# Kernel tuning notes

Measured on AMD Instinct MI355X. Metric: run time of the kernel, lower is better.

## Reference

```python
import jax, jax.numpy as jnp
import numpy as np

N, E = 50000, 800000
H, C_IN, C_HID, C_OUT = 4, 256, 64, 64
NEG_SLOPE = 0.2


def leaky_relu(x, s=NEG_SLOPE):
    return jnp.where(x >= 0, x, s * x)


def gat_conv(x, src, dst, W, att_src, att_dst, bias, n_nodes):
    # x: [N, F_in], W: [F_in, H*C], att_*: [1, H, C], bias: [H*C]
    Hh, Cc = att_src.shape[1], att_src.shape[2]
    h = (x @ W).reshape(n_nodes, Hh, Cc)            # [N, H, C]
    a_src = (h * att_src).sum(-1)                   # [N, H]
    a_dst = (h * att_dst).sum(-1)                   # [N, H]
    alpha = leaky_relu(a_src[src] + a_dst[dst])     # [E, H]
    # segment softmax over incoming edges of each destination node
    m = jax.ops.segment_max(alpha, dst, num_segments=n_nodes)   # [N, H]
    e = jnp.exp(alpha - m[dst])                     # [E, H]
    denom = jax.ops.segment_sum(e, dst, num_segments=n_nodes)   # [N, H]
    w = e / jnp.clip(denom, 1e-16)[dst]             # [E, H]
    out = jax.ops.segment_sum(w[:, :, None] * h[src], dst, num_segments=n_nodes)
    return out.reshape(n_nodes, Hh * Cc) + bias


def setup_inputs() -> dict:
    key = jax.random.key(0)
    ks = jax.random.split(key, 10)
    glorot = lambda k, shp: jax.random.normal(k, shp, jnp.float32) * np.sqrt(2.0 / (shp[0] + shp[-1]))
    return {
        "x": jax.random.normal(ks[0], (N, C_IN), jnp.float32),
        "edge_index": jax.random.randint(ks[1], (2, E), 0, N, jnp.int32),
        "W1": glorot(ks[2], (C_IN, H * C_HID)),
        "att_src1": glorot(ks[3], (1, H, C_HID)),
        "att_dst1": glorot(ks[4], (1, H, C_HID)),
        "b1": jnp.zeros((H * C_HID,), jnp.float32),
        "W2": glorot(ks[5], (H * C_HID, H * C_OUT)),
        "att_src2": glorot(ks[6], (1, H, C_OUT)),
        "att_dst2": glorot(ks[7], (1, H, C_OUT)),
        "b2": jnp.zeros((H * C_OUT,), jnp.float32),
    }


def reference(x, edge_index, W1, att_src1, att_dst1, b1, W2, att_src2, att_dst2, b2):
    n = x.shape[0]
    loops = jnp.arange(n, dtype=edge_index.dtype)
    src = jnp.concatenate([edge_index[0], loops])
    dst = jnp.concatenate([edge_index[1], loops])
    h1 = gat_conv(x, src, dst, W1, att_src1, att_dst1, b1, n)
    h1 = jax.nn.relu(h1)
    out = gat_conv(h1, src, dst, W2, att_src2, att_dst2, b2, n)
    return out
```

## Files before the change

kernel.cpp:

```cpp
#include <hip/hip_runtime.h>
#include <math.h>

#define NEG_SLOPE 0.2f

typedef __attribute__((ext_vector_type(8))) short bf16x8;
typedef __attribute__((ext_vector_type(4))) float f32x4;
typedef __attribute__((ext_vector_type(4))) unsigned short u16x4;
typedef __attribute__((ext_vector_type(8))) unsigned short u16x8;

static __device__ __forceinline__ f32x4 lky4(f32x4 v) {
    f32x4 r;
    r.x = v.x >= 0.f ? v.x : NEG_SLOPE * v.x;
    r.y = v.y >= 0.f ? v.y : NEG_SLOPE * v.y;
    r.z = v.z >= 0.f ? v.z : NEG_SLOPE * v.z;
    r.w = v.w >= 0.f ? v.w : NEG_SLOPE * v.w;
    return r;
}
static __device__ __forceinline__ f32x4 exp4(f32x4 v) {
    f32x4 r;
    r.x = __expf(v.x); r.y = __expf(v.y); r.z = __expf(v.z); r.w = __expf(v.w);
    return r;
}
static __device__ __forceinline__ float bf2f(unsigned short u) {
    return __uint_as_float(((unsigned int)u) << 16);
}
static __device__ __forceinline__ unsigned short f2bf_rne(float f) {
    unsigned int u = __float_as_uint(f);
    u += 0x7fffu + ((u >> 16) & 1u);
    return (unsigned short)(u >> 16);
}


__global__ void hist_kernel(const int* __restrict__ dst, int* __restrict__ counts, int E, int Nn) {
    int i = blockIdx.x * blockDim.x + threadIdx.x;
    int tot = E + Nn;
    if (i < tot) {
        int d = (i < E) ? dst[i] : (i - E);
        atomicAdd(&counts[d], 1);
    }
}

__global__ void scan1_kernel(const int* __restrict__ counts, int* __restrict__ partial,
                             int* __restrict__ blockSums, int Nn) {
    __shared__ int sh[1024];
    int b = blockIdx.x, t = threadIdx.x;
    int base = b * 1024;
    int orig[4];
    for (int r = 0; r < 4; r++) {
        int i = t + r * 256;
        int v = (base + i < Nn) ? counts[base + i] : 0;
        orig[r] = v;
        sh[i] = v;
    }
    __syncthreads();
    for (int off = 1; off < 1024; off <<= 1) {
        int vals[4];
        for (int r = 0; r < 4; r++) { int i = t + r * 256; vals[r] = (i >= off) ? sh[i - off] : 0; }
        __syncthreads();
        for (int r = 0; r < 4; r++) { int i = t + r * 256; sh[i] += vals[r]; }
        __syncthreads();
    }
    for (int r = 0; r < 4; r++) {
        int i = t + r * 256;
        if (base + i < Nn) partial[base + i] = sh[i] - orig[r];
    }
    if (t == 0) blockSums[b] = sh[1023];
}

__global__ void scan2_kernel(int* __restrict__ blockSums, int nb) {
    if (threadIdx.x == 0 && blockIdx.x == 0) {
        int s = 0;
        for (int i = 0; i < nb; i++) { int v = blockSums[i]; blockSums[i] = s; s += v; }
    }
}

__global__ void finalize_kernel(const int* __restrict__ partial, const int* __restrict__ blockOff,
                                int* __restrict__ row_ptr, int Nn, int Etot) {
    int i = blockIdx.x * blockDim.x + threadIdx.x;
    if (i < Nn) row_ptr[i] = partial[i] + blockOff[i >> 10];
    if (i == 0) row_ptr[Nn] = Etot;
}

__global__ void scatter_kernel(const int* __restrict__ srcE, const int* __restrict__ dstE,
                               const int* __restrict__ row_ptr, int* __restrict__ fill,
                               int* __restrict__ srcs, int E, int Nn) {
    int i = blockIdx.x * blockDim.x + threadIdx.x;
    int tot = E + Nn;
    if (i < tot) {
        int s, d;
        if (i < E) { s = srcE[i]; d = dstE[i]; }
        else       { s = d = i - E; }
        int pos = row_ptr[d] + atomicAdd(&fill[d], 1);
        srcs[pos] = s;
    }
}

__global__ void convertA_kernel(const float* __restrict__ X, unsigned short* __restrict__ Ab,
                                int rows) {
    int t = blockIdx.x * 256 + threadIdx.x;
    if (t >= rows * 64) return;
    int r = t >> 6, c4 = t & 63;
    f32x4 v = *((const f32x4*)(X + ((size_t)r << 8)) + c4);
    u16x4 o;
    o.x = f2bf_rne(v.x); o.y = f2bf_rne(v.y);
    o.z = f2bf_rne(v.z); o.w = f2bf_rne(v.w);
    *(u16x4*)(Ab + (size_t)r * 256 + c4 * 4) = o;
}

__global__ void transposeW_kernel(const float* __restrict__ W, unsigned short* __restrict__ Bt) {
    int t = blockIdx.x * 256 + threadIdx.x;
    int n = t >> 8, k = t & 255;
    Bt[(size_t)n * 256 + k] = f2bf_rne(W[k * 256 + n]);
}

__global__ __launch_bounds__(256) void gemm_kernel(const unsigned short* __restrict__ Ab,
                                                   const unsigned short* __restrict__ Bt,
                                                   unsigned short* __restrict__ Gb,
                                                   int rows) {
    __shared__ __align__(128) unsigned char smem[65536];

    int tid = threadIdx.x;
    int lane = tid & 63, wid = tid >> 6;
    int wr = wid >> 1, wc = wid & 1;
    int bm = blockIdx.x * 128;
    int bn = blockIdx.y * 128;

    f32x4 zero4 = {0.f, 0.f, 0.f, 0.f};
    f32x4 acc[4][4];
#pragma unroll
    for (int i = 0; i < 4; i++)
#pragma unroll
        for (int j = 0; j < 4; j++) acc[i][j] = zero4;

    int sr = tid >> 3;
    int sc = tid & 7;

    auto stage = [&](int kt, int buf) {
        unsigned short* As = (unsigned short*)(smem + buf * 32768);
        unsigned short* Bs = As + 8192;
#pragma unroll
        for (int q = 0; q < 4; q++) {
            int rt = q * 32 + sr;
            int gr = bm + rt; if (gr >= rows) gr = rows - 1;
            int cg = sc ^ (rt & 7);
            const unsigned short* gp = Ab + (size_t)gr * 256 + kt + cg * 8;
            unsigned short* lp = As + rt * 64 + sc * 8;
            __builtin_amdgcn_global_load_lds(
                (__attribute__((address_space(1))) void*)(uintptr_t)gp,
                (__attribute__((address_space(3))) void*)lp, 16, 0, 0);
        }
#pragma unroll
        for (int q = 0; q < 4; q++) {
            int rt = q * 32 + sr;
            int gn = bn + rt;
            int cg = sc ^ (rt & 7);
            const unsigned short* gp = Bt + (size_t)gn * 256 + kt + cg * 8;
            unsigned short* lp = Bs + rt * 64 + sc * 8;
            __builtin_amdgcn_global_load_lds(
                (__attribute__((address_space(1))) void*)(uintptr_t)gp,
                (__attribute__((address_space(3))) void*)lp, 16, 0, 0);
        }
    };

    stage(0, 0);
    __syncthreads();

    for (int kt = 0; kt < 4; kt++) {
        if (kt < 3) stage((kt + 1) * 64, (kt + 1) & 1);
        unsigned short* As = (unsigned short*)(smem + (kt & 1) * 32768);
        unsigned short* Bs = As + 8192;
#pragma unroll
        for (int ks = 0; ks < 2; ks++) {
            bf16x8 af[4], bfr[4];
#pragma unroll
            for (int f = 0; f < 4; f++) {
                int r = wr * 64 + f * 16 + (lane & 15);
                int c = (ks * 4 + (lane >> 4)) ^ (r & 7);
                af[f] = *(const bf16x8*)(As + r * 64 + c * 8);
                int rb = wc * 64 + f * 16 + (lane & 15);
                int cb = (ks * 4 + (lane >> 4)) ^ (rb & 7);
                bfr[f] = *(const bf16x8*)(Bs + rb * 64 + cb * 8);
            }
#pragma unroll
            for (int i = 0; i < 4; i++)
#pragma unroll
                for (int j = 0; j < 4; j++)
                    acc[i][j] = __builtin_amdgcn_mfma_f32_16x16x32_bf16(af[i], bfr[j], acc[i][j], 0, 0, 0);
        }
        __syncthreads();
    }

    int r0 = wr * 64 + (lane >> 4) * 4;
    int c0 = wc * 64 + (lane & 15);
#pragma unroll
    for (int i = 0; i < 4; i++) {
#pragma unroll
        for (int j = 0; j < 4; j++) {
#pragma unroll
            for (int rg = 0; rg < 4; rg++) {
                int lr = bm + r0 + i * 16 + rg;
                if (lr < rows) {
                    int col = bn + c0 + j * 16;
                    Gb[(size_t)lr * 256 + col] = f2bf_rne(acc[i][j][rg]);
                }
            }
        }
    }
}

__global__ __launch_bounds__(256) void attn_kernel(const unsigned short* __restrict__ Gb,
                                                   const float* __restrict__ att_s,
                                                   const float* __restrict__ att_d,
                                                   float* __restrict__ a_src,
                                                   float* __restrict__ a_dst, int N) {
    int wv = threadIdx.x >> 6, lane = threadIdx.x & 63;
    int n = blockIdx.x * 4 + wv;
    if (n >= N) return;
    u16x4 g4 = *(const u16x4*)(Gb + (size_t)n * 256 + lane * 4);
    f32x4 g;
    g.x = bf2f(g4.x); g.y = bf2f(g4.y); g.z = bf2f(g4.z); g.w = bf2f(g4.w);
    f32x4 s4 = ((const f32x4*)att_s)[lane];
    f32x4 d4 = ((const f32x4*)att_d)[lane];
    f32x4 p = g * s4, q = g * d4;
    float ps = p.x + p.y + p.z + p.w;
    float pd = q.x + q.y + q.z + q.w;
#pragma unroll
    for (int off = 1; off < 16; off <<= 1) {
        ps += __shfl_xor(ps, off);
        pd += __shfl_xor(pd, off);
    }
    if ((lane & 15) == 0) {
        int head = lane >> 4;
        a_src[n * 4 + head] = ps;
        a_dst[n * 4 + head] = pd;
    }
}

__global__ __launch_bounds__(256) void wts_kernel(const float* __restrict__ a_src,
                                                  const float* __restrict__ a_dst,
                                                  const int* __restrict__ row_ptr,
                                                  const int* __restrict__ srcs,
                                                  float* __restrict__ wts, int N) {
    int wv = threadIdx.x >> 6, lane = threadIdx.x & 63;
    int n = blockIdx.x * 4 + wv;
    if (n >= N) return;
    int start = row_ptr[n], end = row_ptr[n + 1];
    const f32x4* as4p = (const f32x4*)a_src;
    f32x4 adn4 = *(const f32x4*)(a_dst + (size_t)n * 4);

    f32x4 zero = {0.f, 0.f, 0.f, 0.f};
    f32x4 ev0 = zero;
    int e0 = start + lane;
    if (e0 < end) {
        int s = srcs[e0];
        ev0 = exp4(lky4(as4p[s] + adn4));
    }
    f32x4 denom4 = ev0;
    for (int c0 = start + 64; c0 < end; c0 += 64) {
        int e = c0 + lane;
        if (e < end) {
            int s = srcs[e];
            denom4 += exp4(lky4(as4p[s] + adn4));
        }
    }
#pragma unroll
    for (int off = 32; off; off >>= 1) {
        denom4.x += __shfl_xor(denom4.x, off);
        denom4.y += __shfl_xor(denom4.y, off);
        denom4.z += __shfl_xor(denom4.z, off);
        denom4.w += __shfl_xor(denom4.w, off);
    }
    f32x4 rd;
    rd.x = 1.0f / denom4.x; rd.y = 1.0f / denom4.y;
    rd.z = 1.0f / denom4.z; rd.w = 1.0f / denom4.w;

    if (e0 < end) ((f32x4*)wts)[e0] = ev0 * rd;
    for (int c0 = start + 64; c0 < end; c0 += 64) {
        int e = c0 + lane;
        if (e < end) {
            int s = srcs[e];
            ((f32x4*)wts)[e] = exp4(lky4(as4p[s] + adn4)) * rd;
        }
    }
}

__global__ __launch_bounds__(256) void gather_kernel(const unsigned short* __restrict__ Gb,
                                                     const float* __restrict__ wts,
                                                     const int* __restrict__ row_ptr,
                                                     const int* __restrict__ srcs,
                                                     const float* __restrict__ bias,
                                                     float* __restrict__ outF,
                                                     unsigned short* __restrict__ outB,
                                                     int N) {
    int wv = threadIdx.x >> 6, lane = threadIdx.x & 63;
    int n = blockIdx.x * 4 + wv;
    if (n >= N) return;
    int half = lane >> 5;
    int sl = lane & 31;
    int head = sl >> 3;

    int start = row_ptr[n], end = row_ptr[n + 1];

    float acc[8] = {0.f, 0.f, 0.f, 0.f, 0.f, 0.f, 0.f, 0.f};

    int e = start + half;
    for (; e + 2 < end; e += 4) {
        int s0 = srcs[e];
        int s1 = srcs[e + 2];
        float w0 = wts[e * 4 + head];
        float w1 = wts[(e + 2) * 4 + head];
        u16x8 g0 = *(const u16x8*)(Gb + (size_t)s0 * 256 + sl * 8);
        u16x8 g1 = *(const u16x8*)(Gb + (size_t)s1 * 256 + sl * 8);
#pragma unroll
        for (int k = 0; k < 8; k++) {
            acc[k] = fmaf(bf2f(g0[k]), w0, acc[k]);
            acc[k] = fmaf(bf2f(g1[k]), w1, acc[k]);
        }
    }
    for (; e < end; e += 2) {
        int s0 = srcs[e];
        float w0 = wts[e * 4 + head];
        u16x8 g0 = *(const u16x8*)(Gb + (size_t)s0 * 256 + sl * 8);
#pragma unroll
        for (int k = 0; k < 8; k++)
            acc[k] = fmaf(bf2f(g0[k]), w0, acc[k]);
    }

#pragma unroll
    for (int k = 0; k < 8; k++) acc[k] += __shfl_xor(acc[k], 32);

    float r[8];
    const float* bp = bias + sl * 8;
#pragma unroll
    for (int k = 0; k < 8; k++) r[k] = acc[k] + bp[k];

    if (outF) {
        if (half == 0) {
            f32x4 v0 = {r[0], r[1], r[2], r[3]};
            f32x4 v1 = {r[4], r[5], r[6], r[7]};
            f32x4* op = (f32x4*)(outF + (size_t)n * 256 + sl * 8);
            op[0] = v0; op[1] = v1;
        }
    } else {
        if (half == 0) {
            u16x8 v;
#pragma unroll
            for (int k = 0; k < 8; k++) v[k] = f2bf_rne(fmaxf(r[k], 0.f));
            *(u16x8*)(outB + (size_t)n * 256 + sl * 8) = v;
        }
    }
}


extern "C" void kernel_launch(void* const* d_in, const int* in_sizes, int n_in,
                              void* d_out, int out_size, void* d_ws, size_t ws_size,
                              hipStream_t stream) {
    const float* x   = (const float*)d_in[0];
    const int*   ei  = (const int*)d_in[1];
    const float* W1  = (const float*)d_in[2];
    const float* as1 = (const float*)d_in[3];
    const float* ad1 = (const float*)d_in[4];
    const float* b1  = (const float*)d_in[5];
    const float* W2  = (const float*)d_in[6];
    const float* as2 = (const float*)d_in[7];
    const float* ad2 = (const float*)d_in[8];
    const float* b2  = (const float*)d_in[9];

    int N = in_sizes[0] / 256;
    int E = in_sizes[1] / 2;
    int Etot = E + N;
    const int* srcE = ei;
    const int* dstE = ei + E;
    float* out = (float*)d_out;

    char* w = (char*)d_ws;
    size_t used = 0;
    auto alloc = [&](size_t bytes) -> char* {
        char* p = w + used;
        used += (bytes + 255) & ~(size_t)255;
        return p;
    };
    unsigned short* Gb = (unsigned short*)alloc((size_t)N * 256 * 2);
    unsigned short* Ab = (unsigned short*)alloc((size_t)N * 256 * 2);
    float* a_src   = (float*)alloc((size_t)N * 4 * 4);
    float* a_dst   = (float*)alloc((size_t)N * 4 * 4);
    float* wts     = (float*)alloc((size_t)Etot * 4 * 4);
    int* counts    = (int*)alloc((size_t)N * 4);
    int* partial   = (int*)alloc((size_t)N * 4);
    int* row_ptr   = (int*)alloc(((size_t)N + 1) * 4);
    int* srcs      = (int*)alloc((size_t)Etot * 4);
    int* blockSums = (int*)alloc(256 * 4);
    unsigned short* Bt = (unsigned short*)alloc((size_t)256 * 256 * 2);

    hipMemsetAsync(counts, 0, (size_t)N * 4, stream);

    hist_kernel<<<(Etot + 255) / 256, 256, 0, stream>>>(dstE, counts, E, N);
    int nScanBlocks = (N + 1023) / 1024;
    scan1_kernel<<<nScanBlocks, 256, 0, stream>>>(counts, partial, blockSums, N);
    scan2_kernel<<<1, 64, 0, stream>>>(blockSums, nScanBlocks);
    finalize_kernel<<<(N + 255) / 256, 256, 0, stream>>>(partial, blockSums, row_ptr, N, Etot);
    hipMemsetAsync(counts, 0, (size_t)N * 4, stream);
    scatter_kernel<<<(Etot + 255) / 256, 256, 0, stream>>>(srcE, dstE, row_ptr, counts, srcs, E, N);

    int nodeBlocks = (N + 3) / 4;
    dim3 gg((N + 127) / 128, 2);

    convertA_kernel<<<(N * 64 + 255) / 256, 256, 0, stream>>>(x, Ab, N);
    transposeW_kernel<<<256, 256, 0, stream>>>(W1, Bt);
    gemm_kernel<<<gg, 256, 0, stream>>>(Ab, Bt, Gb, N);
    attn_kernel<<<nodeBlocks, 256, 0, stream>>>(Gb, as1, ad1, a_src, a_dst, N);
    wts_kernel<<<nodeBlocks, 256, 0, stream>>>(a_src, a_dst, row_ptr, srcs, wts, N);
    gather_kernel<<<nodeBlocks, 256, 0, stream>>>(Gb, wts, row_ptr, srcs, b1,
                                                  nullptr, Ab, N);

    transposeW_kernel<<<256, 256, 0, stream>>>(W2, Bt);
    gemm_kernel<<<gg, 256, 0, stream>>>(Ab, Bt, Gb, N);
    attn_kernel<<<nodeBlocks, 256, 0, stream>>>(Gb, as2, ad2, a_src, a_dst, N);
    wts_kernel<<<nodeBlocks, 256, 0, stream>>>(a_src, a_dst, row_ptr, srcs, wts, N);
    gather_kernel<<<nodeBlocks, 256, 0, stream>>>(Gb, wts, row_ptr, srcs, b2,
                                                  out, nullptr, N);
}
```

Measured before the change: 326.5 us.

## Fuse attention logits into GEMM epilogue and stage gather indices in LDS

```diff
diff --git a/kernel.cpp b/kernel.cpp
--- a/kernel.cpp
+++ b/kernel.cpp
@@ -116,6 +116,10 @@
 __global__ __launch_bounds__(256) void gemm_kernel(const unsigned short* __restrict__ Ab,
                                                    const unsigned short* __restrict__ Bt,
                                                    unsigned short* __restrict__ Gb,
+                                                   const float* __restrict__ att_s,
+                                                   const float* __restrict__ att_d,
+                                                   float* __restrict__ a_src,
+                                                   float* __restrict__ a_dst,
                                                    int rows) {
     __shared__ __align__(128) unsigned char smem[65536];
 
@@ -206,33 +210,38 @@
             }
         }
     }
-}
-
-__global__ __launch_bounds__(256) void attn_kernel(const unsigned short* __restrict__ Gb,
-                                                   const float* __restrict__ att_s,
-                                                   const float* __restrict__ att_d,
-                                                   float* __restrict__ a_src,
-                                                   float* __restrict__ a_dst, int N) {
-    int wv = threadIdx.x >> 6, lane = threadIdx.x & 63;
-    int n = blockIdx.x * 4 + wv;
-    if (n >= N) return;
-    u16x4 g4 = *(const u16x4*)(Gb + (size_t)n * 256 + lane * 4);
-    f32x4 g;
-    g.x = bf2f(g4.x); g.y = bf2f(g4.y); g.z = bf2f(g4.z); g.w = bf2f(g4.w);
-    f32x4 s4 = ((const f32x4*)att_s)[lane];
-    f32x4 d4 = ((const f32x4*)att_d)[lane];
-    f32x4 p = g * s4, q = g * d4;
-    float ps = p.x + p.y + p.z + p.w;
-    float pd = q.x + q.y + q.z + q.w;
-#pragma unroll
-    for (int off = 1; off < 16; off <<= 1) {
-        ps += __shfl_xor(ps, off);
-        pd += __shfl_xor(pd, off);
-    }
-    if ((lane & 15) == 0) {
-        int head = lane >> 4;
-        a_src[n * 4 + head] = ps;
-        a_dst[n * 4 + head] = pd;
+
+    int head = blockIdx.y * 2 + wc;
+    float atts[4], attd[4];
+#pragma unroll
+    for (int j = 0; j < 4; j++) {
+        int c = bn + c0 + j * 16;
+        atts[j] = att_s[c];
+        attd[j] = att_d[c];
+    }
+#pragma unroll
+    for (int i = 0; i < 4; i++) {
+#pragma unroll
+        for (int rg = 0; rg < 4; rg++) {
+            float s_loc = 0.f, d_loc = 0.f;
+#pragma unroll
+            for (int j = 0; j < 4; j++) {
+                s_loc = fmaf(acc[i][j][rg], atts[j], s_loc);
+                d_loc = fmaf(acc[i][j][rg], attd[j], d_loc);
+            }
+#pragma unroll
+            for (int off = 1; off < 16; off <<= 1) {
+                s_loc += __shfl_xor(s_loc, off);
+                d_loc += __shfl_xor(d_loc, off);
+            }
+            if ((lane & 15) == 0) {
+                int lr = bm + r0 + i * 16 + rg;
+                if (lr < rows) {
+                    a_src[lr * 4 + head] = s_loc;
+                    a_dst[lr * 4 + head] = d_loc;
+                }
+            }
+        }
     }
 }
 
@@ -292,6 +301,8 @@
                                                      float* __restrict__ outF,
                                                      unsigned short* __restrict__ outB,
                                                      int N) {
+    __shared__ int s_lds[4][64];
+    __shared__ f32x4 w_lds[4][64];
     int wv = threadIdx.x >> 6, lane = threadIdx.x & 63;
     int n = blockIdx.x * 4 + wv;
     if (n >= N) return;
@@ -303,27 +314,47 @@
 
     float acc[8] = {0.f, 0.f, 0.f, 0.f, 0.f, 0.f, 0.f, 0.f};
 
-    int e = start + half;
-    for (; e + 2 < end; e += 4) {
-        int s0 = srcs[e];
-        int s1 = srcs[e + 2];
-        float w0 = wts[e * 4 + head];
-        float w1 = wts[(e + 2) * 4 + head];
-        u16x8 g0 = *(const u16x8*)(Gb + (size_t)s0 * 256 + sl * 8);
-        u16x8 g1 = *(const u16x8*)(Gb + (size_t)s1 * 256 + sl * 8);
-#pragma unroll
-        for (int k = 0; k < 8; k++) {
-            acc[k] = fmaf(bf2f(g0[k]), w0, acc[k]);
-            acc[k] = fmaf(bf2f(g1[k]), w1, acc[k]);
-        }
-    }
-    for (; e < end; e += 2) {
-        int s0 = srcs[e];
-        float w0 = wts[e * 4 + head];
-        u16x8 g0 = *(const u16x8*)(Gb + (size_t)s0 * 256 + sl * 8);
-#pragma unroll
-        for (int k = 0; k < 8; k++)
-            acc[k] = fmaf(bf2f(g0[k]), w0, acc[k]);
+    for (int c0 = start; c0 < end; c0 += 64) {
+        int cnt = min(64, end - c0);
+        if (lane < cnt) {
+            s_lds[wv][lane] = srcs[c0 + lane];
+            w_lds[wv][lane] = ((const f32x4*)wts)[c0 + lane];
+        }
+
+        int j = 0;
+        for (; j + 7 < cnt; j += 8) {
+            int e0 = j + half, e1 = j + 2 + half, e2 = j + 4 + half, e3 = j + 6 + half;
+            int s0 = s_lds[wv][e0];
+            int s1 = s_lds[wv][e1];
+            int s2 = s_lds[wv][e2];
+            int s3 = s_lds[wv][e3];
+            float w0 = ((const float*)&w_lds[wv][e0])[head];
+            float w1 = ((const float*)&w_lds[wv][e1])[head];
+            float w2 = ((const float*)&w_lds[wv][e2])[head];
+            float w3 = ((const float*)&w_lds[wv][e3])[head];
+            u16x8 g0 = *(const u16x8*)(Gb + (size_t)s0 * 256 + sl * 8);
+            u16x8 g1 = *(const u16x8*)(Gb + (size_t)s1 * 256 + sl * 8);
+            u16x8 g2 = *(const u16x8*)(Gb + (size_t)s2 * 256 + sl * 8);
+            u16x8 g3 = *(const u16x8*)(Gb + (size_t)s3 * 256 + sl * 8);
+#pragma unroll
+            for (int k = 0; k < 8; k++) {
+                acc[k] = fmaf(bf2f(g0[k]), w0, acc[k]);
+                acc[k] = fmaf(bf2f(g1[k]), w1, acc[k]);
+                acc[k] = fmaf(bf2f(g2[k]), w2, acc[k]);
+                acc[k] = fmaf(bf2f(g3[k]), w3, acc[k]);
+            }
+        }
+        for (; j < cnt; j += 2) {
+            int e = j + half;
+            if (e < cnt) {
+                int s0 = s_lds[wv][e];
+                float w0 = ((const float*)&w_lds[wv][e])[head];
+                u16x8 g0 = *(const u16x8*)(Gb + (size_t)s0 * 256 + sl * 8);
+#pragma unroll
+                for (int k = 0; k < 8; k++)
+                    acc[k] = fmaf(bf2f(g0[k]), w0, acc[k]);
+            }
+        }
     }
 
 #pragma unroll
@@ -407,15 +438,13 @@
 
     convertA_kernel<<<(N * 64 + 255) / 256, 256, 0, stream>>>(x, Ab, N);
     transposeW_kernel<<<256, 256, 0, stream>>>(W1, Bt);
-    gemm_kernel<<<gg, 256, 0, stream>>>(Ab, Bt, Gb, N);
-    attn_kernel<<<nodeBlocks, 256, 0, stream>>>(Gb, as1, ad1, a_src, a_dst, N);
+    gemm_kernel<<<gg, 256, 0, stream>>>(Ab, Bt, Gb, as1, ad1, a_src, a_dst, N);
     wts_kernel<<<nodeBlocks, 256, 0, stream>>>(a_src, a_dst, row_ptr, srcs, wts, N);
     gather_kernel<<<nodeBlocks, 256, 0, stream>>>(Gb, wts, row_ptr, srcs, b1,
                                                   nullptr, Ab, N);
 
     transposeW_kernel<<<256, 256, 0, stream>>>(W2, Bt);
-    gemm_kernel<<<gg, 256, 0, stream>>>(Ab, Bt, Gb, N);
-    attn_kernel<<<nodeBlocks, 256, 0, stream>>>(Gb, as2, ad2, a_src, a_dst, N);
+    gemm_kernel<<<gg, 256, 0, stream>>>(Ab, Bt, Gb, as2, ad2, a_src, a_dst, N);
     wts_kernel<<<nodeBlocks, 256, 0, stream>>>(a_src, a_dst, row_ptr, srcs, wts, N);
     gather_kernel<<<nodeBlocks, 256, 0, stream>>>(Gb, wts, row_ptr, srcs, b2,
                                                   out, nullptr, N);
```

After: 333.9 us. 2.3% more time.

## Fuse softmax weight computation into gather kernel with deferred normalization

Applied to the files above, without the earlier changes.

```diff
diff --git a/kernel.cpp b/kernel.cpp
--- a/kernel.cpp
+++ b/kernel.cpp
@@ -236,62 +236,17 @@
     }
 }
 
-__global__ __launch_bounds__(256) void wts_kernel(const float* __restrict__ a_src,
-                                                  const float* __restrict__ a_dst,
-                                                  const int* __restrict__ row_ptr,
-                                                  const int* __restrict__ srcs,
-                                                  float* __restrict__ wts, int N) {
-    int wv = threadIdx.x >> 6, lane = threadIdx.x & 63;
-    int n = blockIdx.x * 4 + wv;
-    if (n >= N) return;
-    int start = row_ptr[n], end = row_ptr[n + 1];
-    const f32x4* as4p = (const f32x4*)a_src;
-    f32x4 adn4 = *(const f32x4*)(a_dst + (size_t)n * 4);
-
-    f32x4 zero = {0.f, 0.f, 0.f, 0.f};
-    f32x4 ev0 = zero;
-    int e0 = start + lane;
-    if (e0 < end) {
-        int s = srcs[e0];
-        ev0 = exp4(lky4(as4p[s] + adn4));
-    }
-    f32x4 denom4 = ev0;
-    for (int c0 = start + 64; c0 < end; c0 += 64) {
-        int e = c0 + lane;
-        if (e < end) {
-            int s = srcs[e];
-            denom4 += exp4(lky4(as4p[s] + adn4));
-        }
-    }
-#pragma unroll
-    for (int off = 32; off; off >>= 1) {
-        denom4.x += __shfl_xor(denom4.x, off);
-        denom4.y += __shfl_xor(denom4.y, off);
-        denom4.z += __shfl_xor(denom4.z, off);
-        denom4.w += __shfl_xor(denom4.w, off);
-    }
-    f32x4 rd;
-    rd.x = 1.0f / denom4.x; rd.y = 1.0f / denom4.y;
-    rd.z = 1.0f / denom4.z; rd.w = 1.0f / denom4.w;
-
-    if (e0 < end) ((f32x4*)wts)[e0] = ev0 * rd;
-    for (int c0 = start + 64; c0 < end; c0 += 64) {
-        int e = c0 + lane;
-        if (e < end) {
-            int s = srcs[e];
-            ((f32x4*)wts)[e] = exp4(lky4(as4p[s] + adn4)) * rd;
-        }
-    }
-}
-
 __global__ __launch_bounds__(256) void gather_kernel(const unsigned short* __restrict__ Gb,
-                                                     const float* __restrict__ wts,
+                                                     const float* __restrict__ a_src,
+                                                     const float* __restrict__ a_dst,
                                                      const int* __restrict__ row_ptr,
                                                      const int* __restrict__ srcs,
                                                      const float* __restrict__ bias,
                                                      float* __restrict__ outF,
                                                      unsigned short* __restrict__ outB,
                                                      int N) {
+    __shared__ int s_lds[4][64];
+    __shared__ f32x4 w_lds[4][64];
     int wv = threadIdx.x >> 6, lane = threadIdx.x & 63;
     int n = blockIdx.x * 4 + wv;
     if (n >= N) return;
@@ -300,39 +255,74 @@
     int head = sl >> 3;
 
     int start = row_ptr[n], end = row_ptr[n + 1];
+    const f32x4* as4p = (const f32x4*)a_src;
+    f32x4 adn4 = *(const f32x4*)(a_dst + (size_t)n * 4);
 
     float acc[8] = {0.f, 0.f, 0.f, 0.f, 0.f, 0.f, 0.f, 0.f};
-
-    int e = start + half;
-    for (; e + 2 < end; e += 4) {
-        int s0 = srcs[e];
-        int s1 = srcs[e + 2];
-        float w0 = wts[e * 4 + head];
-        float w1 = wts[(e + 2) * 4 + head];
-        u16x8 g0 = *(const u16x8*)(Gb + (size_t)s0 * 256 + sl * 8);
-        u16x8 g1 = *(const u16x8*)(Gb + (size_t)s1 * 256 + sl * 8);
-#pragma unroll
-        for (int k = 0; k < 8; k++) {
-            acc[k] = fmaf(bf2f(g0[k]), w0, acc[k]);
-            acc[k] = fmaf(bf2f(g1[k]), w1, acc[k]);
-        }
-    }
-    for (; e < end; e += 2) {
-        int s0 = srcs[e];
-        float w0 = wts[e * 4 + head];
-        u16x8 g0 = *(const u16x8*)(Gb + (size_t)s0 * 256 + sl * 8);
-#pragma unroll
-        for (int k = 0; k < 8; k++)
-            acc[k] = fmaf(bf2f(g0[k]), w0, acc[k]);
+    f32x4 dsum4 = {0.f, 0.f, 0.f, 0.f};
+
+    for (int c0 = start; c0 < end; c0 += 64) {
+        int cnt = min(64, end - c0);
+        if (lane < cnt) {
+            int s = srcs[c0 + lane];
+            f32x4 ev = exp4(lky4(as4p[s] + adn4));
+            s_lds[wv][lane] = s;
+            w_lds[wv][lane] = ev;
+            dsum4 += ev;
+        }
+
+        int j = 0;
+        for (; j + 7 < cnt; j += 8) {
+            int e0 = j + half, e1 = j + 2 + half, e2 = j + 4 + half, e3 = j + 6 + half;
+            int s0 = s_lds[wv][e0];
+            int s1 = s_lds[wv][e1];
+            int s2 = s_lds[wv][e2];
+            int s3 = s_lds[wv][e3];
+            float w0 = ((const float*)&w_lds[wv][e0])[head];
+            float w1 = ((const float*)&w_lds[wv][e1])[head];
+            float w2 = ((const float*)&w_lds[wv][e2])[head];
+            float w3 = ((const float*)&w_lds[wv][e3])[head];
+            u16x8 g0 = *(const u16x8*)(Gb + (size_t)s0 * 256 + sl * 8);
+            u16x8 g1 = *(const u16x8*)(Gb + (size_t)s1 * 256 + sl * 8);
+            u16x8 g2 = *(const u16x8*)(Gb + (size_t)s2 * 256 + sl * 8);
+            u16x8 g3 = *(const u16x8*)(Gb + (size_t)s3 * 256 + sl * 8);
+#pragma unroll
+            for (int k = 0; k < 8; k++) {
+                acc[k] = fmaf(bf2f(g0[k]), w0, acc[k]);
+                acc[k] = fmaf(bf2f(g1[k]), w1, acc[k]);
+                acc[k] = fmaf(bf2f(g2[k]), w2, acc[k]);
+                acc[k] = fmaf(bf2f(g3[k]), w3, acc[k]);
+            }
+        }
+        for (; j < cnt; j += 2) {
+            int e = j + half;
+            if (e < cnt) {
+                int s0 = s_lds[wv][e];
+                float w0 = ((const float*)&w_lds[wv][e])[head];
+                u16x8 g0 = *(const u16x8*)(Gb + (size_t)s0 * 256 + sl * 8);
+#pragma unroll
+                for (int k = 0; k < 8; k++)
+                    acc[k] = fmaf(bf2f(g0[k]), w0, acc[k]);
+            }
+        }
     }
 
 #pragma unroll
     for (int k = 0; k < 8; k++) acc[k] += __shfl_xor(acc[k], 32);
+#pragma unroll
+    for (int off = 32; off; off >>= 1) {
+        dsum4.x += __shfl_xor(dsum4.x, off);
+        dsum4.y += __shfl_xor(dsum4.y, off);
+        dsum4.z += __shfl_xor(dsum4.z, off);
+        dsum4.w += __shfl_xor(dsum4.w, off);
+    }
+    float den = head == 0 ? dsum4.x : head == 1 ? dsum4.y : head == 2 ? dsum4.z : dsum4.w;
+    float rden = 1.0f / den;
 
     float r[8];
     const float* bp = bias + sl * 8;
 #pragma unroll
-    for (int k = 0; k < 8; k++) r[k] = acc[k] + bp[k];
+    for (int k = 0; k < 8; k++) r[k] = acc[k] * rden + bp[k];
 
     if (outF) {
         if (half == 0) {
@@ -384,7 +374,6 @@
     unsigned short* Ab = (unsigned short*)alloc((size_t)N * 256 * 2);
     float* a_src   = (float*)alloc((size_t)N * 4 * 4);
     float* a_dst   = (float*)alloc((size_t)N * 4 * 4);
-    float* wts     = (float*)alloc((size_t)Etot * 4 * 4);
     int* counts    = (int*)alloc((size_t)N * 4);
     int* partial   = (int*)alloc((size_t)N * 4);
     int* row_ptr   = (int*)alloc(((size_t)N + 1) * 4);
@@ -409,14 +398,12 @@
     transposeW_kernel<<<256, 256, 0, stream>>>(W1, Bt);
     gemm_kernel<<<gg, 256, 0, stream>>>(Ab, Bt, Gb, N);
     attn_kernel<<<nodeBlocks, 256, 0, stream>>>(Gb, as1, ad1, a_src, a_dst, N);
-    wts_kernel<<<nodeBlocks, 256, 0, stream>>>(a_src, a_dst, row_ptr, srcs, wts, N);
-    gather_kernel<<<nodeBlocks, 256, 0, stream>>>(Gb, wts, row_ptr, srcs, b1,
+    gather_kernel<<<nodeBlocks, 256, 0, stream>>>(Gb, a_src, a_dst, row_ptr, srcs, b1,
                                                   nullptr, Ab, N);
 
     transposeW_kernel<<<256, 256, 0, stream>>>(W2, Bt);
     gemm_kernel<<<gg, 256, 0, stream>>>(Ab, Bt, Gb, N);
     attn_kernel<<<nodeBlocks, 256, 0, stream>>>(Gb, as2, ad2, a_src, a_dst, N);
-    wts_kernel<<<nodeBlocks, 256, 0, stream>>>(a_src, a_dst, row_ptr, srcs, wts, N);
-    gather_kernel<<<nodeBlocks, 256, 0, stream>>>(Gb, wts, row_ptr, srcs, b2,
+    gather_kernel<<<nodeBlocks, 256, 0, stream>>>(Gb, a_src, a_dst, row_ptr, srcs, b2,
                                                   out, nullptr, N);
 }
```

Result: faster. 301.0 us (-7.8%).
